# Performance work log

Hardware: AMD Instinct MI355X
Metric: run time of the kernel (lower is better)

## Reference

```python
import jax, jax.numpy as jnp
import numpy as np

B, T, D_IN, D_OUT = 16, 2048, 2048, 2048
N_ADAPTERS, RANK = 8, 16


def setup_inputs() -> dict:
    key = jax.random.key(0)
    k_x, k_w, k_a, k_b, k_s, k_idx = jax.random.split(key, 6)
    x = jax.random.normal(k_x, (B, T, D_IN), dtype=jnp.float32)
    # frozen base weight (nn.Linear stores W as (d_out, d_in)); bias=False
    W = jax.random.normal(k_w, (D_OUT, D_IN), dtype=jnp.float32) * (1.0 / np.sqrt(D_IN))
    # stacked adapter bank: A[a] is (r, d_in), Bm[a] is (d_out, r)
    A = jax.random.normal(k_a, (N_ADAPTERS, RANK, D_IN), dtype=jnp.float32) * 0.02
    Bm = jax.random.normal(k_b, (N_ADAPTERS, D_OUT, RANK), dtype=jnp.float32) * 0.02
    scalings = jnp.ones((N_ADAPTERS,), dtype=jnp.float32)  # alpha / r, pre-merged
    adapter_idx = jax.random.randint(k_idx, (B,), 0, N_ADAPTERS, dtype=jnp.int32)
    return {"x": x, "W": W, "A": A, "Bm": Bm, "scalings": scalings,
            "adapter_idx": adapter_idx}


def reference(x, W, A, Bm, scalings, adapter_idx):
    # base path: H = x @ W^T   -> (B, T, d_out)
    H = jnp.einsum("btd,od->bto", x, W)
    # per-request adapter gather (replaces the Python loop over adapter groups)
    A_b = A[adapter_idx]          # (B, r, d_in)
    B_b = Bm[adapter_idx]         # (B, d_out, r)
    s_b = scalings[adapter_idx]   # (B,)
    # low-rank delta: (x @ A^T) @ B^T, done per request, fully batched
    xa = jnp.einsum("btd,brd->btr", x, A_b)        # (B, T, r)
    delta = jnp.einsum("btr,bor->bto", xa, B_b)    # (B, T, d_out)
    # original computes delta under torch.no_grad() with detached A/B
    delta = jax.lax.stop_gradient(delta * s_b[:, None, None])
    return H + delta
```

## Files before the change

kernel.cpp:

```cpp
#include <hip/hip_runtime.h>
#include <stdint.h>

typedef unsigned short u16;
typedef __attribute__((ext_vector_type(4))) short s16x4;
typedef __attribute__((ext_vector_type(8))) short short8;
typedef __attribute__((ext_vector_type(4))) float f32x4;

static __device__ __forceinline__ u16 f2bf(float f) {
    union { float f; uint32_t u; } c; c.f = f;
    uint32_t u = c.u;
    u += 0x7FFFu + ((u >> 16) & 1u);
    return (u16)(u >> 16);
}

#define D_IN   2048
#define D_OUT  2048
#define MTOT   32768
#define BK     64
#define NTM    32

__device__ __forceinline__ void gload16(const u16* g, u16* l) {
    __builtin_amdgcn_global_load_lds(
        (const __attribute__((address_space(1))) void*)g,
        (__attribute__((address_space(3))) void*)l, 16, 0, 0);
}

__global__ __launch_bounds__(256) void k_pre(
    const float* __restrict__ x, const float* __restrict__ W,
    const float* __restrict__ A, const float* __restrict__ Bm,
    const float* __restrict__ scal, const int* __restrict__ aidx,
    u16* __restrict__ xb, u16* __restrict__ Wb, u16* __restrict__ Bp,
    u16* __restrict__ xa)
{
    __shared__ __align__(16) u16 Xs[32 * BK];
    __shared__ __align__(16) u16 Ps[64 * BK];
    const int b = blockIdx.x, tid = threadIdx.x;

    if (b >= 1024) {
        if (b < 3072) {
            int i = ((b - 1024) * 256 + tid) * 8;
            const float4* p = (const float4*)(W + i);
            float4 v0 = p[0], v1 = p[1];
            short8 o;
            o[0]=f2bf(v0.x); o[1]=f2bf(v0.y); o[2]=f2bf(v0.z); o[3]=f2bf(v0.w);
            o[4]=f2bf(v1.x); o[5]=f2bf(v1.y); o[6]=f2bf(v1.z); o[7]=f2bf(v1.w);
            *(short8*)(Wb + i) = o;
        } else {
            int i = (b - 3072) * 256 + tid;
            int j = i & 63, n = (i >> 6) & 2047, a = i >> 17;
            Bp[i] = (j < 16) ? f2bf(Bm[((((a << 11) + n)) << 4) + j]) : (u16)0;
        }
        return;
    }

    const int lane = tid & 63, wid = tid >> 6;
    const int m0 = b << 5;
    const int a = aidx[m0 >> 11];
    const float s = scal[a];
    const int wr = wid >> 1, wc = wid & 1;
    const int arow = (wr << 4) + (lane & 15);
    const int brow = (wc << 5) + (lane & 15);

    f32x4 acc[2];
    acc[0] = 0.f; acc[1] = 0.f;

    {
        s16x4 z; z[0]=0; z[1]=0; z[2]=0; z[3]=0;
        #pragma unroll
        for (int j = 0; j < 3; ++j)
            *(s16x4*)(Ps + 1024 + tid * 12 + j * 4) = z;
    }

    const int xrow_l = tid >> 4;
    const int xcol   = (tid & 15) << 2;
    const int wslot  = (tid & 15) >> 1;
    const int wsub   = (tid & 1) << 2;
    const int prow  = tid >> 4;
    const int pcolg = tid & 15;
    const float* Arow = A + ((size_t)((a << 4) + prow) << 11) + (pcolg << 2);
    u16* pdst = Ps + (prow << 6) + ((((pcolg >> 1) ^ (prow & 7))) << 3) + ((pcolg & 1) << 2);

    for (int kt = 0; kt < NTM; ++kt) {
        const int k0 = kt << 6;
        float4 xv[2];
        #pragma unroll
        for (int j = 0; j < 2; ++j)
            xv[j] = *(const float4*)(x + ((size_t)(m0 + (j << 4) + xrow_l) << 11) + k0 + xcol);
        float4 av = *(const float4*)(Arow + k0);
        #pragma unroll
        for (int j = 0; j < 2; ++j) {
            const int row = (j << 4) + xrow_l;
            s16x4 c4;
            c4[0]=f2bf(xv[j].x); c4[1]=f2bf(xv[j].y); c4[2]=f2bf(xv[j].z); c4[3]=f2bf(xv[j].w);
            *(s16x4*)(Xs + (row << 6) + ((wslot ^ (row & 7)) << 3) + wsub) = c4;
            *(s16x4*)(xb + ((size_t)(m0 + row) << 11) + k0 + xcol) = c4;
        }
        {
            s16x4 a4;
            a4[0]=f2bf(av.x); a4[1]=f2bf(av.y); a4[2]=f2bf(av.z); a4[3]=f2bf(av.w);
            *(s16x4*)pdst = a4;
        }
        __syncthreads();
        #pragma unroll
        for (int kk = 0; kk < 2; ++kk) {
            const int sl = ((kk << 2) + (lane >> 4)) ^ (lane & 7);
            short8 af = *(const short8*)(Xs + (arow << 6) + (sl << 3));
            #pragma unroll
            for (int ni = 0; ni < 2; ++ni) {
                short8 bv = *(const short8*)(Ps + ((brow + ni * 16) << 6) + (sl << 3));
                acc[ni] = __builtin_amdgcn_mfma_f32_16x16x32_bf16(af, bv, acc[ni], 0, 0, 0);
            }
        }
        __syncthreads();
    }

    #pragma unroll
    for (int ni = 0; ni < 2; ++ni) {
        const int cc = (wc << 5) + ni * 16 + (lane & 15);
        #pragma unroll
        for (int rr = 0; rr < 4; ++rr) {
            const int mm = m0 + (wr << 4) + ((lane >> 4) << 2) + rr;
            xa[((size_t)mm << 6) + cc] = f2bf(acc[ni][rr] * s);
        }
    }
}

__global__ __launch_bounds__(512, 2) void k_gemm(
    const u16* __restrict__ xb, const u16* __restrict__ Wb,
    const u16* __restrict__ xa, const u16* __restrict__ Bp,
    const int* __restrict__ aidx, float* __restrict__ out)
{
    __shared__ __align__(16) u16 LDS[2 * 32768];
    const int tid = threadIdx.x, lane = tid & 63, wid = tid >> 6;

    const int newbid = (blockIdx.x & 7) * 128 + (blockIdx.x >> 3);
    const int bm = newbid >> 3, bn = newbid & 7;
    const int m0 = bm << 8, n0 = bn << 8;
    const int wr = wid >> 2, wc = wid & 3;
    const int a = aidx[m0 >> 11];

    f32x4 acc[8][4];
    #pragma unroll
    for (int i = 0; i < 8; ++i)
        #pragma unroll
        for (int j = 0; j < 4; ++j) acc[i][j] = 0.0f;

    const int sc = ((tid & 7) ^ ((tid >> 3) & 7)) << 3;
    const int srw = tid >> 3;

    const int sl0 = (((lane >> 4)    ) ^ (lane & 7)) << 3;
    const int sl1 = (((lane >> 4) + 4) ^ (lane & 7)) << 3;
    const int aRowBase = (wr << 7) + (lane & 15);
    const int bRowBase = (wc << 6) + (lane & 15);

    short8 af[4][2], bv[4][2];

    auto STG = [&](const u16* ptr, int stride, int rowbase, int kofs, int ldsofs) {
        const u16* s_ = ptr + ((size_t)(rowbase + srw)) * stride + kofs + sc;
        gload16(s_,                          &LDS[ldsofs + (tid << 3)]);
        gload16(s_ + ((size_t)stride << 6),  &LDS[ldsofs + 4096 + (tid << 3)]);
    };
    auto SA = [&](int tt, int h) {
        const int lo = ((tt & 1) << 15) + (h << 13);
        if (tt < NTM) STG(xb, 2048, m0 + (h << 7), tt << 6, lo);
        else          STG(xa, 64,   m0 + (h << 7), 0,       lo);
    };
    auto SB = [&](int tt, int h) {
        const int lo = ((tt & 1) << 15) + 16384 + (h << 13);
        if (tt < NTM) STG(Wb, 2048, n0 + (h << 7), tt << 6, lo);
        else          STG(Bp, 64,   (a << 11) + n0 + (h << 7), 0, lo);
    };

    #define BAR  __builtin_amdgcn_s_barrier()
    #define LGK0 do { asm volatile("s_waitcnt lgkmcnt(0)" ::: "memory"); \
                      __builtin_amdgcn_sched_barrier(0); } while (0)

    #define RDA(c_, mq_) do { _Pragma("unroll")                                     \
        for (int mi = 0; mi < 4; ++mi) {                                            \
            const int row = aRowBase + ((mq_) << 6) + (mi << 4);                    \
            af[mi][0] = *(const short8*)&LDS[((c_) << 15) + (row << 6) + sl0];      \
            af[mi][1] = *(const short8*)&LDS[((c_) << 15) + (row << 6) + sl1];      \
        } } while (0)

    #define RDB(c_, ni_) do {                                                       \
            const int row = bRowBase + ((ni_) << 4);                                \
            bv[ni_][0] = *(const short8*)&LDS[((c_) << 15) + 16384 + (row << 6) + sl0]; \
            bv[ni_][1] = *(const short8*)&LDS[((c_) << 15) + 16384 + (row << 6) + sl1]; \
        } while (0)

    #define MM(mq_, ns_) do { __builtin_amdgcn_s_setprio(1); _Pragma("unroll")      \
        for (int kk = 0; kk < 2; ++kk) _Pragma("unroll")                            \
        for (int mi = 0; mi < 4; ++mi) _Pragma("unroll")                            \
        for (int j = 0; j < 2; ++j)                                                 \
            acc[(mq_) * 4 + mi][(ns_) * 2 + j] =                                    \
                __builtin_amdgcn_mfma_f32_16x16x32_bf16(af[mi][kk],                 \
                    bv[(ns_) * 2 + j][kk], acc[(mq_) * 4 + mi][(ns_) * 2 + j], 0, 0, 0); \
        __builtin_amdgcn_s_setprio(0); } while (0)

    SA(0, 0); SA(0, 1); SB(0, 0); SB(0, 1); SB(1, 0); SB(1, 1);
    asm volatile("s_waitcnt vmcnt(4)" ::: "memory");
    BAR;

    for (int t = 0; t <= NTM; ++t) {
        const int c = t & 1;
        RDB(c, 0); RDB(c, 1); RDA(c, 0);
        if (t + 1 <= NTM) SA(t + 1, 0);
        BAR; LGK0; MM(0, 0); BAR;
        RDB(c, 2); RDB(c, 3);
        if (t + 1 <= NTM) SA(t + 1, 1);
        BAR; LGK0; MM(0, 1); BAR;
        RDA(c, 1);
        if (t + 2 <= NTM) SB(t + 2, 0);
        BAR; LGK0; MM(1, 0); BAR;
        if (t + 2 <= NTM) SB(t + 2, 1);
        BAR; MM(1, 1);
        if (t < NTM - 1)      asm volatile("s_waitcnt vmcnt(4)" ::: "memory");
        else if (t == NTM - 1) asm volatile("s_waitcnt vmcnt(0)" ::: "memory");
        BAR;
    }

    #undef MM
    #undef RDB
    #undef RDA
    #undef LGK0
    #undef BAR

    #pragma unroll
    for (int mi = 0; mi < 8; ++mi) {
        #pragma unroll
        for (int ni = 0; ni < 4; ++ni) {
            const int nn = n0 + (wc << 6) + ni * 16 + (lane & 15);
            #pragma unroll
            for (int r = 0; r < 4; ++r) {
                const int mm = m0 + (wr << 7) + mi * 16 + ((lane >> 4) << 2) + r;
                out[((size_t)mm << 11) + nn] = acc[mi][ni][r];
            }
        }
    }
}

extern "C" void kernel_launch(void* const* d_in, const int* in_sizes, int n_in,
                              void* d_out, int out_size, void* d_ws, size_t ws_size,
                              hipStream_t stream) {
    const float* x  = (const float*)d_in[0];
    const float* W  = (const float*)d_in[1];
    const float* A  = (const float*)d_in[2];
    const float* Bm = (const float*)d_in[3];
    const float* sc = (const float*)d_in[4];
    const int* aidx = (const int*)d_in[5];
    float* out = (float*)d_out;

    char* ws = (char*)d_ws;
    u16* xb = (u16*)(ws);
    u16* Wb = (u16*)(ws + 134217728);
    u16* Bp = (u16*)(ws + 134217728 + 8388608 + 2097152);
    u16* xa = (u16*)(ws + 134217728 + 8388608 + 2097152 + 2097152);

    hipLaunchKernelGGL(k_pre,  dim3(7168), dim3(256), 0, stream,
                       x, W, A, Bm, sc, aidx, xb, Wb, Bp, xa);
    hipLaunchKernelGGL(k_gemm, dim3(1024), dim3(512), 0, stream,
                       xb, Wb, xa, Bp, aidx, out);
}
```

Measured before the change: 369.7 us.

## Reorder GEMM inner loop to split by k-half and swap A/B prefetch depth

Restructures the per-tile MFMA schedule so that each of the four phases computes a full 4x4 sub-block over one k-half, rather than over a quarter of the N columns. A fragments for both M halves are kept live in separate registers and B is read per k-half. The A and B roles in the staging pipeline are swapped: B is now prefetched one tile ahead and A two tiles ahead. The aim is a better overlap of LDS reads and global loads with MFMA work, at the cost of more live fragment registers.

```diff
diff --git a/kernel.cpp b/kernel.cpp
--- a/kernel.cpp
+++ b/kernel.cpp
@@ -153,7 +153,7 @@
     const int aRowBase = (wr << 7) + (lane & 15);
     const int bRowBase = (wc << 6) + (lane & 15);
 
-    short8 af[4][2], bv[4][2];
+    short8 af0[4][2], af1[4][2], bv0[4], bv1[4];
 
     auto STG = [&](const u16* ptr, int stride, int rowbase, int kofs, int ldsofs) {
         const u16* s_ = ptr + ((size_t)(rowbase + srw)) * stride + kofs + sc;
@@ -175,46 +175,44 @@
     #define LGK0 do { asm volatile("s_waitcnt lgkmcnt(0)" ::: "memory"); \
                       __builtin_amdgcn_sched_barrier(0); } while (0)
 
-    #define RDA(c_, mq_) do { _Pragma("unroll")                                     \
+    #define RDA(dst, c_, mq_) do { _Pragma("unroll")                                \
         for (int mi = 0; mi < 4; ++mi) {                                            \
             const int row = aRowBase + ((mq_) << 6) + (mi << 4);                    \
-            af[mi][0] = *(const short8*)&LDS[((c_) << 15) + (row << 6) + sl0];      \
-            af[mi][1] = *(const short8*)&LDS[((c_) << 15) + (row << 6) + sl1];      \
+            dst[mi][0] = *(const short8*)&LDS[((c_) << 15) + (row << 6) + sl0];     \
+            dst[mi][1] = *(const short8*)&LDS[((c_) << 15) + (row << 6) + sl1];     \
         } } while (0)
 
-    #define RDB(c_, ni_) do {                                                       \
-            const int row = bRowBase + ((ni_) << 4);                                \
-            bv[ni_][0] = *(const short8*)&LDS[((c_) << 15) + 16384 + (row << 6) + sl0]; \
-            bv[ni_][1] = *(const short8*)&LDS[((c_) << 15) + 16384 + (row << 6) + sl1]; \
-        } while (0)
-
-    #define MM(mq_, ns_) do { __builtin_amdgcn_s_setprio(1); _Pragma("unroll")      \
-        for (int kk = 0; kk < 2; ++kk) _Pragma("unroll")                            \
+    #define RDB(dst, c_, slx) do { _Pragma("unroll")                                \
+        for (int ni = 0; ni < 4; ++ni) {                                            \
+            const int row = bRowBase + (ni << 4);                                   \
+            dst[ni] = *(const short8*)&LDS[((c_) << 15) + 16384 + (row << 6) + (slx)]; \
+        } } while (0)
+
+    #define MM(afA, bvA, kkI, mq_) do { __builtin_amdgcn_s_setprio(1); _Pragma("unroll") \
         for (int mi = 0; mi < 4; ++mi) _Pragma("unroll")                            \
-        for (int j = 0; j < 2; ++j)                                                 \
-            acc[(mq_) * 4 + mi][(ns_) * 2 + j] =                                    \
-                __builtin_amdgcn_mfma_f32_16x16x32_bf16(af[mi][kk],                 \
-                    bv[(ns_) * 2 + j][kk], acc[(mq_) * 4 + mi][(ns_) * 2 + j], 0, 0, 0); \
+        for (int ni = 0; ni < 4; ++ni)                                              \
+            acc[(mq_) * 4 + mi][ni] = __builtin_amdgcn_mfma_f32_16x16x32_bf16(      \
+                afA[mi][kkI], bvA[ni], acc[(mq_) * 4 + mi][ni], 0, 0, 0);           \
         __builtin_amdgcn_s_setprio(0); } while (0)
 
-    SA(0, 0); SA(0, 1); SB(0, 0); SB(0, 1); SB(1, 0); SB(1, 1);
+    SA(0, 0); SA(0, 1); SB(0, 0); SB(0, 1); SA(1, 0); SA(1, 1);
     asm volatile("s_waitcnt vmcnt(4)" ::: "memory");
     BAR;
 
     for (int t = 0; t <= NTM; ++t) {
         const int c = t & 1;
-        RDB(c, 0); RDB(c, 1); RDA(c, 0);
-        if (t + 1 <= NTM) SA(t + 1, 0);
-        BAR; LGK0; MM(0, 0); BAR;
-        RDB(c, 2); RDB(c, 3);
-        if (t + 1 <= NTM) SA(t + 1, 1);
-        BAR; LGK0; MM(0, 1); BAR;
-        RDA(c, 1);
-        if (t + 2 <= NTM) SB(t + 2, 0);
-        BAR; LGK0; MM(1, 0); BAR;
-        if (t + 2 <= NTM) SB(t + 2, 1);
-        BAR; MM(1, 1);
-        if (t < NTM - 1)      asm volatile("s_waitcnt vmcnt(4)" ::: "memory");
+        RDA(af0, c, 0); RDB(bv0, c, sl0);
+        if (t + 1 <= NTM) SB(t + 1, 0);
+        BAR; LGK0; MM(af0, bv0, 0, 0); BAR;
+        RDA(af1, c, 1);
+        if (t + 1 <= NTM) SB(t + 1, 1);
+        BAR; LGK0; MM(af1, bv0, 0, 1); BAR;
+        RDB(bv1, c, sl1);
+        if (t + 2 <= NTM) SA(t + 2, 0);
+        BAR; LGK0; MM(af0, bv1, 1, 0); BAR;
+        if (t + 2 <= NTM) SA(t + 2, 1);
+        BAR; MM(af1, bv1, 1, 1);
+        if (t < NTM - 1)       asm volatile("s_waitcnt vmcnt(4)" ::: "memory");
         else if (t == NTM - 1) asm volatile("s_waitcnt vmcnt(0)" ::: "memory");
         BAR;
     }
```

Result: no change. 376.0 us (+1.7%).
